# Kernel tuning notes

Measured on AMD Instinct MI355X. Metric: run time of the kernel, lower is better.

The kernel has to match this reference:

```python
import jax, jax.numpy as jnp
import numpy as np

N = 10000      # nodes per stream graph
DIN = 128      # dim_in
DH = 512       # dim_h (== 256 * n_inputs, required by the head-input bug)
E = 160000     # edges per stream (before self-loops)
DOUT = 16      # dim_out
EPS = 1e-5     # BatchNorm eps

def _init(k, shape, fan):
    return jax.random.normal(k, shape, jnp.float32) * (1.0 / np.sqrt(fan))

def setup_inputs():
    key = jax.random.key(0)
    ks = iter(jax.random.split(key, 32))
    inp = {}
    for s in range(2):
        inp[f"data{s}"] = jax.random.normal(next(ks), (N, DIN), jnp.float32)
        inp[f"edge_index{s}"] = jax.random.randint(next(ks), (2, E), 0, N)
        inp[f"batch{s}"] = jnp.sort(jax.random.randint(next(ks), (N,), 0, 32))
        # GATv2Conv params (heads=1, concat): lin_l, lin_r, att, out-bias
        inp[f"Wl{s}"] = _init(next(ks), (DIN, DH), DIN)
        inp[f"bl{s}"] = jnp.zeros((DH,), jnp.float32)
        inp[f"Wr{s}"] = _init(next(ks), (DIN, DH), DIN)
        inp[f"br{s}"] = jnp.zeros((DH,), jnp.float32)
        inp[f"att{s}"] = _init(next(ks), (DH,), DH)
        inp[f"bias{s}"] = jnp.zeros((DH,), jnp.float32)
        inp[f"gamma{s}"] = jnp.ones((DH,), jnp.float32)
        inp[f"beta{s}"] = jnp.zeros((DH,), jnp.float32)
    inp["W1"] = _init(next(ks), (512, 256), 512); inp["b1"] = jnp.zeros((256,), jnp.float32)
    inp["g1"] = jnp.ones((256,), jnp.float32); inp["be1"] = jnp.zeros((256,), jnp.float32)
    inp["W2"] = _init(next(ks), (256, 128), 256); inp["b2"] = jnp.zeros((128,), jnp.float32)
    inp["g2"] = jnp.ones((128,), jnp.float32); inp["be2"] = jnp.zeros((128,), jnp.float32)
    inp["W3"] = _init(next(ks), (128, DOUT), 128); inp["b3"] = jnp.zeros((DOUT,), jnp.float32)
    inp["train"] = 0
    return inp

def _gatv2(x, Wl, bl, Wr, br, att, bias, src, dst):
    # PyG GATv2Conv (heads=1, negative_slope=0.2, self-loops already in src/dst)
    xl = x @ Wl + bl                                    # [N, DH] source transform
    xr = x @ Wr + br                                    # [N, DH] target transform
    logits = jax.nn.leaky_relu(xl[src] + xr[dst], 0.2) @ att   # [E+N]
    m = jax.ops.segment_max(logits, dst, num_segments=N)
    ex = jnp.exp(logits - m[dst])
    den = jax.ops.segment_sum(ex, dst, num_segments=N)
    alpha = ex / den[dst]                               # edge softmax over incoming edges
    out = jax.ops.segment_sum(xl[src] * alpha[:, None], dst, num_segments=N)
    return out + bias

def _bn(h, g, b):
    # BatchNorm1d in training mode (module never set to eval): batch stats, biased var
    mu = h.mean(0)
    v = ((h - mu) ** 2).mean(0)
    return g * (h - mu) * jax.lax.rsqrt(v + EPS) + b

def _forward(data0, Wl0, bl0, Wr0, br0, att0, bias0, gamma0, beta0,
             data1, Wl1, bl1, Wr1, br1, att1, bias1, gamma1, beta1,
             W1, b1, g1, be1, W2, b2, g2, be2, W3, b3,
             edge_index0, edge_index1):
    loops = jnp.arange(N)
    streams = [
        (data0, edge_index0, Wl0, bl0, Wr0, br0, att0, bias0, gamma0, beta0),
        (data1, edge_index1, Wl1, bl1, Wr1, br1, att1, bias1, gamma1, beta1),
    ]
    h = None
    for (x, ei, Wl, bl, Wr, br, att, bias, g, b) in streams:
        src = jnp.concatenate([ei[0], loops])   # PyG adds self-loops by default
        dst = jnp.concatenate([ei[1], loops])
        # source bug `i / 2 == 0`: only the FIRST conv+BN of each stream executes
        h = jax.nn.relu(_gatv2(x, Wl, bl, Wr, br, att, bias, src, dst))
        h = _bn(h, g, b)
        # dropout(p=0.1) inactive: train=False (eval)
    # source bug: head consumes last-stream node features `h`, not pooled h_out
    z = jax.nn.relu(h @ W1 + b1)
    z = _bn(z, g1, be1)
    z = jax.nn.relu(z @ W2 + b2)
    z = _bn(z, g2, be2)
    z = z @ W3 + b3
    return jax.nn.sigmoid(z), jax.nn.log_softmax(z, axis=1)

def reference(data0, edge_index0, batch0, Wl0, bl0, Wr0, br0, att0, bias0, gamma0, beta0,
              data1, edge_index1, batch1, Wl1, bl1, Wr1, br1, att1, bias1, gamma1, beta1,
              W1, b1, g1, be1, W2, b2, g2, be2, W3, b3, train):
    return _forward(data0, Wl0, bl0, Wr0, br0, att0, bias0, gamma0, beta0,
                    data1, Wl1, bl1, Wr1, br1, att1, bias1, gamma1, beta1,
                    W1, b1, g1, be1, W2, b2, g2, be2, W3, b3,
                    edge_index0, edge_index1)
```

## Files before the change

kernel.cpp:

```cpp
#include <hip/hip_runtime.h>
#include <cmath>

#define NN 10000
#define DINX 128
#define DHX 512
#define EE 160000
#define TOTE (EE + NN)
#define DOUTX 16
#define BN_EPS 1e-5f

template <bool RELU, bool BNA>
__global__ void gemm_kernel(const float* __restrict__ A, const float* __restrict__ B,
                            const float* __restrict__ bias,
                            const float* __restrict__ sA, const float* __restrict__ tA,
                            float* __restrict__ C, int M, int K, int Nn) {
    __shared__ float As[32][68];
    __shared__ float Bs[32][68];
    const int t = threadIdx.x;
    const int tx = t & 15, ty = t >> 4;
    const int mBase = blockIdx.y * 64;
    const int nBase = blockIdx.x * 64;
    float acc[4][4] = {};
    for (int k0 = 0; k0 < K; k0 += 32) {
        #pragma unroll
        for (int i = 0; i < 2; i++) {
            int idx = t + i * 256;
            int r = idx >> 3;
            int c4 = idx & 7;
            int gm = mBase + r;
            int kc = k0 + c4 * 4;
            float4 v = {0.f, 0.f, 0.f, 0.f};
            if (gm < M) v = *(const float4*)&A[(size_t)gm * K + kc];
            if (BNA) {
                v.x = v.x * sA[kc + 0] + tA[kc + 0];
                v.y = v.y * sA[kc + 1] + tA[kc + 1];
                v.z = v.z * sA[kc + 2] + tA[kc + 2];
                v.w = v.w * sA[kc + 3] + tA[kc + 3];
            }
            As[c4 * 4 + 0][r] = v.x;
            As[c4 * 4 + 1][r] = v.y;
            As[c4 * 4 + 2][r] = v.z;
            As[c4 * 4 + 3][r] = v.w;
        }
        #pragma unroll
        for (int i = 0; i < 2; i++) {
            int idx = t + i * 256;
            int kr = idx >> 4;
            int nc4 = idx & 15;
            int gn = nBase + nc4 * 4;
            float4 v = {0.f, 0.f, 0.f, 0.f};
            if (gn + 3 < Nn) v = *(const float4*)&B[(size_t)(k0 + kr) * Nn + gn];
            *(float4*)&Bs[kr][nc4 * 4] = v;
        }
        __syncthreads();
        #pragma unroll
        for (int kk = 0; kk < 32; kk++) {
            float4 a = *(const float4*)&As[kk][ty * 4];
            float4 b = *(const float4*)&Bs[kk][tx * 4];
            float av[4] = {a.x, a.y, a.z, a.w};
            float bv[4] = {b.x, b.y, b.z, b.w};
            #pragma unroll
            for (int i = 0; i < 4; i++)
                #pragma unroll
                for (int j = 0; j < 4; j++) acc[i][j] += av[i] * bv[j];
        }
        __syncthreads();
    }
    const int gn0 = nBase + tx * 4;
    #pragma unroll
    for (int i = 0; i < 4; i++) {
        int gm = mBase + ty * 4 + i;
        if (gm >= M) continue;
        if (gn0 + 3 < Nn) {
            float4 v;
            v.x = acc[i][0] + bias[gn0 + 0];
            v.y = acc[i][1] + bias[gn0 + 1];
            v.z = acc[i][2] + bias[gn0 + 2];
            v.w = acc[i][3] + bias[gn0 + 3];
            if (RELU) {
                v.x = fmaxf(v.x, 0.f); v.y = fmaxf(v.y, 0.f);
                v.z = fmaxf(v.z, 0.f); v.w = fmaxf(v.w, 0.f);
            }
            *(float4*)&C[(size_t)gm * Nn + gn0] = v;
        } else {
            #pragma unroll
            for (int j = 0; j < 4; j++) {
                int gn = gn0 + j;
                if (gn >= Nn) continue;
                float v = acc[i][j] + bias[gn];
                if (RELU) v = fmaxf(v, 0.f);
                C[(size_t)gm * Nn + gn] = v;
            }
        }
    }
}

__global__ void deg_kernel(const int* __restrict__ dst, int* __restrict__ deg) {
    int i = blockIdx.x * 256 + threadIdx.x;
    if (i >= TOTE) return;
    int d = (i < EE) ? dst[i] : (i - EE);
    atomicAdd(&deg[d], 1);
}

#define SCAN_PER 10
__global__ void scan_kernel(const int* __restrict__ deg, int* __restrict__ off,
                            int* __restrict__ cur, int n) {
    const int t = threadIdx.x;
    const int lane = t & 63, w = t >> 6;
    const int base = t * SCAN_PER;
    int v[SCAN_PER];
    int s = 0;
    #pragma unroll
    for (int i = 0; i < SCAN_PER; i++) {
        int idx = base + i;
        int d = (idx < n) ? deg[idx] : 0;
        s += d;
        v[i] = s;
    }
    int x = s;
    #pragma unroll
    for (int sh = 1; sh < 64; sh <<= 1) {
        int y = __shfl_up(x, sh, 64);
        if (lane >= sh) x += y;
    }
    __shared__ int wsum[16];
    if (lane == 63) wsum[w] = x;
    __syncthreads();
    int wpre = 0;
    for (int i = 0; i < w; i++) wpre += wsum[i];
    const int excl = wpre + x - s;
    #pragma unroll
    for (int i = 0; i < SCAN_PER; i++) {
        int idx = base + i;
        if (idx < n) {
            off[idx + 1] = excl + v[i];
            cur[idx] = excl + (i ? v[i - 1] : 0);
        }
    }
    if (t == 0) off[0] = 0;
}

__global__ void scatter_kernel(const int* __restrict__ src, const int* __restrict__ dst,
                               int* __restrict__ cur, int* __restrict__ csr) {
    int i = blockIdx.x * 256 + threadIdx.x;
    if (i >= TOTE) return;
    int s = (i < EE) ? src[i] : (i - EE);
    int d = (i < EE) ? dst[i] : (i - EE);
    int pos = atomicAdd(&cur[d], 1);
    csr[pos] = s;
}

#define GAT_WPB 4
__global__ void gat_node_kernel(const float* __restrict__ xl, const float* __restrict__ xr,
                                const float* __restrict__ att, const float* __restrict__ bias,
                                const int* __restrict__ off, const int* __restrict__ csr,
                                float* __restrict__ h) {
    const int wave = threadIdx.x >> 6;
    const int lane = threadIdx.x & 63;
    const int n = blockIdx.x * GAT_WPB + wave;
    if (n >= NN) return;

    const float4* xr4 = (const float4*)(xr + (size_t)n * DHX);
    const float4* att4 = (const float4*)att;
    const float4 xr0 = xr4[lane],      xr1 = xr4[lane + 64];
    const float4 at0 = att4[lane],     at1 = att4[lane + 64];

    const int o0 = off[n], o1 = off[n + 1];

    float4 a0 = {0.f, 0.f, 0.f, 0.f}, a1 = {0.f, 0.f, 0.f, 0.f};
    float m = -INFINITY, den = 0.f;

    for (int e = o0; e < o1; e++) {
        const int s = csr[e];
        const float4* x4 = (const float4*)(xl + (size_t)s * DHX);
        const float4 x0 = x4[lane], x1 = x4[lane + 64];
        float v;
        {
            float4 l0, l1;
            l0.x = x0.x + xr0.x; l0.y = x0.y + xr0.y; l0.z = x0.z + xr0.z; l0.w = x0.w + xr0.w;
            l1.x = x1.x + xr1.x; l1.y = x1.y + xr1.y; l1.z = x1.z + xr1.z; l1.w = x1.w + xr1.w;
            l0.x = (l0.x > 0.f) ? l0.x : 0.2f * l0.x;
            l0.y = (l0.y > 0.f) ? l0.y : 0.2f * l0.y;
            l0.z = (l0.z > 0.f) ? l0.z : 0.2f * l0.z;
            l0.w = (l0.w > 0.f) ? l0.w : 0.2f * l0.w;
            l1.x = (l1.x > 0.f) ? l1.x : 0.2f * l1.x;
            l1.y = (l1.y > 0.f) ? l1.y : 0.2f * l1.y;
            l1.z = (l1.z > 0.f) ? l1.z : 0.2f * l1.z;
            l1.w = (l1.w > 0.f) ? l1.w : 0.2f * l1.w;
            v  = l0.x * at0.x + l0.y * at0.y + l0.z * at0.z + l0.w * at0.w;
            v += l1.x * at1.x + l1.y * at1.y + l1.z * at1.z + l1.w * at1.w;
        }
        #pragma unroll
        for (int sft = 32; sft; sft >>= 1) v += __shfl_xor(v, sft, 64);
        if (v > m) {
            const float r = expf(m - v);
            den *= r;
            a0.x *= r; a0.y *= r; a0.z *= r; a0.w *= r;
            a1.x *= r; a1.y *= r; a1.z *= r; a1.w *= r;
            m = v;
        }
        const float p = expf(v - m);
        den += p;
        a0.x += p * x0.x; a0.y += p * x0.y; a0.z += p * x0.z; a0.w += p * x0.w;
        a1.x += p * x1.x; a1.y += p * x1.y; a1.z += p * x1.z; a1.w += p * x1.w;
    }

    const float inv = 1.f / den;
    const float4 b0 = ((const float4*)bias)[lane];
    const float4 b1 = ((const float4*)bias)[lane + 64];
    float4 o0v, o1v;
    o0v.x = fmaxf(a0.x * inv + b0.x, 0.f);
    o0v.y = fmaxf(a0.y * inv + b0.y, 0.f);
    o0v.z = fmaxf(a0.z * inv + b0.z, 0.f);
    o0v.w = fmaxf(a0.w * inv + b0.w, 0.f);
    o1v.x = fmaxf(a1.x * inv + b1.x, 0.f);
    o1v.y = fmaxf(a1.y * inv + b1.y, 0.f);
    o1v.z = fmaxf(a1.z * inv + b1.z, 0.f);
    o1v.w = fmaxf(a1.w * inv + b1.w, 0.f);
    float4* h4 = (float4*)(h + (size_t)n * DHX);
    h4[lane] = o0v;
    h4[lane + 64] = o1v;
}

#define BN_GRID 625
template <int C>
__global__ void bn_stats_kernel(const float* __restrict__ x, float* __restrict__ partial) {
    constexpr int G = C / 4;
    constexpr int S = 256 / G;
    constexpr int IT = 16 / S;
    const int t = threadIdx.x;
    const int cg = t & (G - 1);
    const int sub = t / G;
    const size_t r0 = (size_t)blockIdx.x * 16 + sub;
    float4 s = {0.f, 0.f, 0.f, 0.f}, q = {0.f, 0.f, 0.f, 0.f};
    #pragma unroll
    for (int i = 0; i < IT; i++) {
        const float4 v = *(const float4*)&x[(r0 + (size_t)i * S) * C + cg * 4];
        s.x += v.x; s.y += v.y; s.z += v.z; s.w += v.w;
        q.x += v.x * v.x; q.y += v.y * v.y; q.z += v.z * v.z; q.w += v.w * v.w;
    }
    __shared__ float ls[2048];
    float* lsub = ls + sub * 2 * C;
    *(float4*)&lsub[cg * 4] = s;
    *(float4*)&lsub[C + cg * 4] = q;
    __syncthreads();
    for (int k = t; k < 2 * C; k += 256) {
        float acc = 0.f;
        #pragma unroll
        for (int ss = 0; ss < S; ss++) acc += ls[ss * 2 * C + k];
        partial[(size_t)blockIdx.x * 2 * C + k] = acc;
    }
}

template <int C>
__global__ void bn_affine_kernel(const float* __restrict__ partial,
                                 const float* __restrict__ g, const float* __restrict__ b,
                                 float* __restrict__ scale, float* __restrict__ shift,
                                 float invM) {
    const int c = blockIdx.x;
    const int t = threadIdx.x;
    float s = 0.f, q = 0.f;
    for (int p = t; p < BN_GRID; p += 256) {
        s += partial[(size_t)p * 2 * C + c];
        q += partial[(size_t)p * 2 * C + C + c];
    }
    #pragma unroll
    for (int sh = 32; sh; sh >>= 1) {
        s += __shfl_xor(s, sh, 64);
        q += __shfl_xor(q, sh, 64);
    }
    __shared__ float ws[8];
    const int lane = t & 63, w = t >> 6;
    if (lane == 0) { ws[w] = s; ws[4 + w] = q; }
    __syncthreads();
    if (t == 0) {
        s = ws[0] + ws[1] + ws[2] + ws[3];
        q = ws[4] + ws[5] + ws[6] + ws[7];
        float mu = s * invM;
        float var = q * invM - mu * mu;
        float sc = g[c] * rsqrtf(var + BN_EPS);
        scale[c] = sc;
        shift[c] = b[c] - mu * sc;
    }
}

__global__ void head_out_kernel(const float* __restrict__ z3, float* __restrict__ out, int M) {
    int r = blockIdx.x * 256 + threadIdx.x;
    if (r >= M) return;
    float v[DOUTX];
    float mx = -INFINITY;
    #pragma unroll
    for (int i = 0; i < DOUTX; i++) { v[i] = z3[(size_t)r * DOUTX + i]; mx = fmaxf(mx, v[i]); }
    float s = 0.f;
    #pragma unroll
    for (int i = 0; i < DOUTX; i++) s += expf(v[i] - mx);
    float lse = mx + logf(s);
    #pragma unroll
    for (int i = 0; i < DOUTX; i++) out[(size_t)r * DOUTX + i] = 1.f / (1.f + expf(-v[i]));
    #pragma unroll
    for (int i = 0; i < DOUTX; i++) out[(size_t)(M * DOUTX) + (size_t)r * DOUTX + i] = v[i] - lse;
}

extern "C" void kernel_launch(void* const* d_in, const int* in_sizes, int n_in,
                              void* d_out, int out_size, void* d_ws, size_t ws_size,
                              hipStream_t stream) {
    const float* data1  = (const float*)d_in[11];
    const int*   ei1    = (const int*)d_in[12];
    const float* Wl1    = (const float*)d_in[14];
    const float* bl1    = (const float*)d_in[15];
    const float* Wr1    = (const float*)d_in[16];
    const float* br1    = (const float*)d_in[17];
    const float* att1   = (const float*)d_in[18];
    const float* bias1  = (const float*)d_in[19];
    const float* gamma1 = (const float*)d_in[20];
    const float* beta1  = (const float*)d_in[21];
    const float* W1  = (const float*)d_in[22];
    const float* b1  = (const float*)d_in[23];
    const float* g1  = (const float*)d_in[24];
    const float* be1 = (const float*)d_in[25];
    const float* W2  = (const float*)d_in[26];
    const float* b2  = (const float*)d_in[27];
    const float* g2  = (const float*)d_in[28];
    const float* be2 = (const float*)d_in[29];
    const float* W3  = (const float*)d_in[30];
    const float* b3  = (const float*)d_in[31];

    const int* e_src = ei1;
    const int* e_dst = ei1 + EE;

    float* fws = (float*)d_ws;
    float* xl = fws;
    float* xr = fws + 5120000;
    float* h  = fws + 10240000;
    int* ibase = (int*)(fws + 15360000);
    int* deg   = ibase;
    int* offs  = ibase + 10000;
    int* cur   = ibase + 20016;
    int* csr   = ibase + 30016;
    float* scale   = fws + 15625600;
    float* shift   = fws + 15626112;
    float* z1 = xr;
    float* z2 = xl;
    float* z3 = xl + 4000000;
    float* part_h  = xl;
    float* part_z1 = xl;
    float* part_z2 = h;
    float* out = (float*)d_out;

    dim3 blk(256);

    dim3 gg(DHX / 64, (NN + 63) / 64);
    hipLaunchKernelGGL((gemm_kernel<false, false>), gg, blk, 0, stream, data1, Wl1, bl1, nullptr, nullptr, xl, NN, DINX, DHX);
    hipLaunchKernelGGL((gemm_kernel<false, false>), gg, blk, 0, stream, data1, Wr1, br1, nullptr, nullptr, xr, NN, DINX, DHX);

    hipMemsetAsync(deg, 0, NN * sizeof(int), stream);
    hipLaunchKernelGGL(deg_kernel, dim3((TOTE + 255) / 256), blk, 0, stream, e_dst, deg);
    hipLaunchKernelGGL(scan_kernel, dim3(1), dim3(1024), 0, stream, deg, offs, cur, NN);
    hipLaunchKernelGGL(scatter_kernel, dim3((TOTE + 255) / 256), blk, 0, stream, e_src, e_dst, cur, csr);

    hipLaunchKernelGGL(gat_node_kernel, dim3((NN + GAT_WPB - 1) / GAT_WPB), blk, 0, stream,
                       xl, xr, att1, bias1, offs, csr, h);

    hipLaunchKernelGGL((bn_stats_kernel<512>), dim3(BN_GRID), blk, 0, stream, h, part_h);
    hipLaunchKernelGGL((bn_affine_kernel<512>), dim3(512), blk, 0, stream, part_h, gamma1, beta1, scale, shift, 1.f / NN);

    hipLaunchKernelGGL((gemm_kernel<true, true>), dim3(256 / 64, (NN + 63) / 64), blk, 0, stream, h, W1, b1, scale, shift, z1, NN, 512, 256);
    hipLaunchKernelGGL((bn_stats_kernel<256>), dim3(BN_GRID), blk, 0, stream, z1, part_z1);
    hipLaunchKernelGGL((bn_affine_kernel<256>), dim3(256), blk, 0, stream, part_z1, g1, be1, scale, shift, 1.f / NN);

    hipLaunchKernelGGL((gemm_kernel<true, true>), dim3(128 / 64, (NN + 63) / 64), blk, 0, stream, z1, W2, b2, scale, shift, z2, NN, 256, 128);
    hipLaunchKernelGGL((bn_stats_kernel<128>), dim3(BN_GRID), blk, 0, stream, z2, part_z2);
    hipLaunchKernelGGL((bn_affine_kernel<128>), dim3(128), blk, 0, stream, part_z2, g2, be2, scale, shift, 1.f / NN);

    hipLaunchKernelGGL((gemm_kernel<false, true>), dim3(1, (NN + 63) / 64), blk, 0, stream, z2, W3, b3, scale, shift, z3, NN, 128, DOUTX);
    hipLaunchKernelGGL(head_out_kernel, dim3((NN + 255) / 256), blk, 0, stream, z3, out, NN);

    (void)in_sizes; (void)n_in; (void)out_size; (void)ws_size;
}
```

Before: 372.4 us.

## Enlarge GEMM tiles to 128 rows with swizzled block order, prefetch GAT neighbor rows

The GEMM now computes 128x64 tiles with 8x4 accumulators per thread, which doubles A-tile reuse per loaded B element. It uses a 1D grid that groups blocks in sets of 8 M-strips per N column, likely to improve L2 reuse. The GAT aggregation loop now loads the next neighbor's feature row before computing on the current one, to hide gather latency. The costs are higher register pressure, fewer blocks for the small head GEMMs, and fewer waves per SM.

```diff
diff --git a/kernel.cpp b/kernel.cpp
--- a/kernel.cpp
+++ b/kernel.cpp
@@ -10,20 +10,30 @@
 #define BN_EPS 1e-5f
 
 template <bool RELU, bool BNA>
-__global__ void gemm_kernel(const float* __restrict__ A, const float* __restrict__ B,
-                            const float* __restrict__ bias,
-                            const float* __restrict__ sA, const float* __restrict__ tA,
-                            float* __restrict__ C, int M, int K, int Nn) {
-    __shared__ float As[32][68];
+__global__ void gemm3_kernel(const float* __restrict__ A, const float* __restrict__ B,
+                             const float* __restrict__ bias,
+                             const float* __restrict__ sA, const float* __restrict__ tA,
+                             float* __restrict__ C, int M, int K, int Nn,
+                             int mB, int nB) {
+    const int bid = blockIdx.x;
+    const int x = bid & 7;
+    const int rest = bid >> 3;
+    const int sg = rest / nB;
+    const int nblk = rest - sg * nB;
+    const int mstrip = x + (sg << 3);
+    if (mstrip >= mB) return;
+    const int mBase = mstrip * 128;
+    const int nBase = nblk * 64;
+
+    __shared__ float As[32][132];
     __shared__ float Bs[32][68];
     const int t = threadIdx.x;
     const int tx = t & 15, ty = t >> 4;
-    const int mBase = blockIdx.y * 64;
-    const int nBase = blockIdx.x * 64;
-    float acc[4][4] = {};
+
+    float acc[8][4] = {};
     for (int k0 = 0; k0 < K; k0 += 32) {
         #pragma unroll
-        for (int i = 0; i < 2; i++) {
+        for (int i = 0; i < 4; i++) {
             int idx = t + i * 256;
             int r = idx >> 3;
             int c4 = idx & 7;
@@ -55,12 +65,13 @@
         __syncthreads();
         #pragma unroll
         for (int kk = 0; kk < 32; kk++) {
-            float4 a = *(const float4*)&As[kk][ty * 4];
-            float4 b = *(const float4*)&Bs[kk][tx * 4];
-            float av[4] = {a.x, a.y, a.z, a.w};
+            float4 a0 = *(const float4*)&As[kk][ty * 8];
+            float4 a1 = *(const float4*)&As[kk][ty * 8 + 4];
+            float4 b  = *(const float4*)&Bs[kk][tx * 4];
+            float av[8] = {a0.x, a0.y, a0.z, a0.w, a1.x, a1.y, a1.z, a1.w};
             float bv[4] = {b.x, b.y, b.z, b.w};
             #pragma unroll
-            for (int i = 0; i < 4; i++)
+            for (int i = 0; i < 8; i++)
                 #pragma unroll
                 for (int j = 0; j < 4; j++) acc[i][j] += av[i] * bv[j];
         }
@@ -68,8 +79,8 @@
     }
     const int gn0 = nBase + tx * 4;
     #pragma unroll
-    for (int i = 0; i < 4; i++) {
-        int gm = mBase + ty * 4 + i;
+    for (int i = 0; i < 8; i++) {
+        int gm = mBase + ty * 8 + i;
         if (gm >= M) continue;
         if (gn0 + 3 < Nn) {
             float4 v;
@@ -170,39 +181,49 @@
     float4 a0 = {0.f, 0.f, 0.f, 0.f}, a1 = {0.f, 0.f, 0.f, 0.f};
     float m = -INFINITY, den = 0.f;
 
-    for (int e = o0; e < o1; e++) {
-        const int s = csr[e];
-        const float4* x4 = (const float4*)(xl + (size_t)s * DHX);
-        const float4 x0 = x4[lane], x1 = x4[lane + 64];
-        float v;
-        {
-            float4 l0, l1;
-            l0.x = x0.x + xr0.x; l0.y = x0.y + xr0.y; l0.z = x0.z + xr0.z; l0.w = x0.w + xr0.w;
-            l1.x = x1.x + xr1.x; l1.y = x1.y + xr1.y; l1.z = x1.z + xr1.z; l1.w = x1.w + xr1.w;
-            l0.x = (l0.x > 0.f) ? l0.x : 0.2f * l0.x;
-            l0.y = (l0.y > 0.f) ? l0.y : 0.2f * l0.y;
-            l0.z = (l0.z > 0.f) ? l0.z : 0.2f * l0.z;
-            l0.w = (l0.w > 0.f) ? l0.w : 0.2f * l0.w;
-            l1.x = (l1.x > 0.f) ? l1.x : 0.2f * l1.x;
-            l1.y = (l1.y > 0.f) ? l1.y : 0.2f * l1.y;
-            l1.z = (l1.z > 0.f) ? l1.z : 0.2f * l1.z;
-            l1.w = (l1.w > 0.f) ? l1.w : 0.2f * l1.w;
-            v  = l0.x * at0.x + l0.y * at0.y + l0.z * at0.z + l0.w * at0.w;
-            v += l1.x * at1.x + l1.y * at1.y + l1.z * at1.z + l1.w * at1.w;
-        }
-        #pragma unroll
-        for (int sft = 32; sft; sft >>= 1) v += __shfl_xor(v, sft, 64);
-        if (v > m) {
-            const float r = expf(m - v);
-            den *= r;
-            a0.x *= r; a0.y *= r; a0.z *= r; a0.w *= r;
-            a1.x *= r; a1.y *= r; a1.z *= r; a1.w *= r;
-            m = v;
-        }
-        const float p = expf(v - m);
-        den += p;
-        a0.x += p * x0.x; a0.y += p * x0.y; a0.z += p * x0.z; a0.w += p * x0.w;
-        a1.x += p * x1.x; a1.y += p * x1.y; a1.z += p * x1.z; a1.w += p * x1.w;
+    {
+        const int s0 = csr[o0];
+        const float4* p0 = (const float4*)(xl + (size_t)s0 * DHX);
+        a0 = a0;
+        float4 nx0 = p0[lane], nx1 = p0[lane + 64];
+        for (int e = o0; e < o1; e++) {
+            const float4 x0 = nx0, x1 = nx1;
+            if (e + 1 < o1) {
+                const int s2 = csr[e + 1];
+                const float4* p2 = (const float4*)(xl + (size_t)s2 * DHX);
+                nx0 = p2[lane];
+                nx1 = p2[lane + 64];
+            }
+            float v;
+            {
+                float4 l0, l1;
+                l0.x = x0.x + xr0.x; l0.y = x0.y + xr0.y; l0.z = x0.z + xr0.z; l0.w = x0.w + xr0.w;
+                l1.x = x1.x + xr1.x; l1.y = x1.y + xr1.y; l1.z = x1.z + xr1.z; l1.w = x1.w + xr1.w;
+                l0.x = (l0.x > 0.f) ? l0.x : 0.2f * l0.x;
+                l0.y = (l0.y > 0.f) ? l0.y : 0.2f * l0.y;
+                l0.z = (l0.z > 0.f) ? l0.z : 0.2f * l0.z;
+                l0.w = (l0.w > 0.f) ? l0.w : 0.2f * l0.w;
+                l1.x = (l1.x > 0.f) ? l1.x : 0.2f * l1.x;
+                l1.y = (l1.y > 0.f) ? l1.y : 0.2f * l1.y;
+                l1.z = (l1.z > 0.f) ? l1.z : 0.2f * l1.z;
+                l1.w = (l1.w > 0.f) ? l1.w : 0.2f * l1.w;
+                v  = l0.x * at0.x + l0.y * at0.y + l0.z * at0.z + l0.w * at0.w;
+                v += l1.x * at1.x + l1.y * at1.y + l1.z * at1.z + l1.w * at1.w;
+            }
+            #pragma unroll
+            for (int sft = 32; sft; sft >>= 1) v += __shfl_xor(v, sft, 64);
+            if (v > m) {
+                const float r = expf(m - v);
+                den *= r;
+                a0.x *= r; a0.y *= r; a0.z *= r; a0.w *= r;
+                a1.x *= r; a1.y *= r; a1.z *= r; a1.w *= r;
+                m = v;
+            }
+            const float p = expf(v - m);
+            den += p;
+            a0.x += p * x0.x; a0.y += p * x0.y; a0.z += p * x0.z; a0.w += p * x0.w;
+            a1.x += p * x1.x; a1.y += p * x1.y; a1.z += p * x1.z; a1.w += p * x1.w;
+        }
     }
 
     const float inv = 1.f / den;
@@ -348,10 +369,13 @@
     float* out = (float*)d_out;
 
     dim3 blk(256);
-
-    dim3 gg(DHX / 64, (NN + 63) / 64);
-    hipLaunchKernelGGL((gemm_kernel<false, false>), gg, blk, 0, stream, data1, Wl1, bl1, nullptr, nullptr, xl, NN, DINX, DHX);
-    hipLaunchKernelGGL((gemm_kernel<false, false>), gg, blk, 0, stream, data1, Wr1, br1, nullptr, nullptr, xr, NN, DINX, DHX);
+    const int mB = (NN + 127) / 128;
+    const int sgc = (mB + 7) / 8;
+
+    hipLaunchKernelGGL((gemm3_kernel<false, false>), dim3(8 * sgc * 8), blk, 0, stream,
+                       data1, Wl1, bl1, nullptr, nullptr, xl, NN, DINX, DHX, mB, 8);
+    hipLaunchKernelGGL((gemm3_kernel<false, false>), dim3(8 * sgc * 8), blk, 0, stream,
+                       data1, Wr1, br1, nullptr, nullptr, xr, NN, DINX, DHX, mB, 8);
 
     hipMemsetAsync(deg, 0, NN * sizeof(int), stream);
     hipLaunchKernelGGL(deg_kernel, dim3((TOTE + 255) / 256), blk, 0, stream, e_dst, deg);
@@ -364,15 +388,18 @@
     hipLaunchKernelGGL((bn_stats_kernel<512>), dim3(BN_GRID), blk, 0, stream, h, part_h);
     hipLaunchKernelGGL((bn_affine_kernel<512>), dim3(512), blk, 0, stream, part_h, gamma1, beta1, scale, shift, 1.f / NN);
 
-    hipLaunchKernelGGL((gemm_kernel<true, true>), dim3(256 / 64, (NN + 63) / 64), blk, 0, stream, h, W1, b1, scale, shift, z1, NN, 512, 256);
+    hipLaunchKernelGGL((gemm3_kernel<true, true>), dim3(8 * sgc * 4), blk, 0, stream,
+                       h, W1, b1, scale, shift, z1, NN, 512, 256, mB, 4);
     hipLaunchKernelGGL((bn_stats_kernel<256>), dim3(BN_GRID), blk, 0, stream, z1, part_z1);
     hipLaunchKernelGGL((bn_affine_kernel<256>), dim3(256), blk, 0, stream, part_z1, g1, be1, scale, shift, 1.f / NN);
 
-    hipLaunchKernelGGL((gemm_kernel<true, true>), dim3(128 / 64, (NN + 63) / 64), blk, 0, stream, z1, W2, b2, scale, shift, z2, NN, 256, 128);
+    hipLaunchKernelGGL((gemm3_kernel<true, true>), dim3(8 * sgc * 2), blk, 0, stream,
+                       z1, W2, b2, scale, shift, z2, NN, 256, 128, mB, 2);
     hipLaunchKernelGGL((bn_stats_kernel<128>), dim3(BN_GRID), blk, 0, stream, z2, part_z2);
     hipLaunchKernelGGL((bn_affine_kernel<128>), dim3(128), blk, 0, stream, part_z2, g2, be2, scale, shift, 1.f / NN);
 
-    hipLaunchKernelGGL((gemm_kernel<false, true>), dim3(1, (NN + 63) / 64), blk, 0, stream, z2, W3, b3, scale, shift, z3, NN, 128, DOUTX);
+    hipLaunchKernelGGL((gemm3_kernel<false, true>), dim3(8 * sgc * 1), blk, 0, stream,
+                       z2, W3, b3, scale, shift, z3, NN, 128, DOUTX, mB, 1);
     hipLaunchKernelGGL(head_out_kernel, dim3((NN + 255) / 256), blk, 0, stream, z3, out, NN);
 
     (void)in_sizes; (void)n_in; (void)out_size; (void)ws_size;
```

New measurement: 395.4 us. 6.2% more time.
